# Kernel optimization log

Hardware: AMD Instinct MI355X
Metric: run time of the kernel (lower is better)

## Reference

```python
import jax, jax.numpy as jnp
import numpy as np

EPS = 1e-8
N_REFINE = 10
LR_REFINE = 0.1
N_SAMPLES = 12
M_BLEND = 0.3      # self.m
MARGIN = 0.2
TAU = 0.07
USE_INFONCE = True


def safe_norm(x, axis=-1):
    return x / jnp.clip(jnp.linalg.norm(x, axis=axis, keepdims=True), EPS, None)


def setup_inputs() -> dict:
    key = jax.random.key(0)
    k1, k2, k3, k4 = jax.random.split(key, 4)
    K, C, N, H, W = 10, 768, 8, 64, 64
    fg_proto = safe_norm(jax.random.normal(k1, (K, C), jnp.float32))
    bg_proto = safe_norm(jax.random.normal(k2, (K, C), jnp.float32))
    F_map = jax.random.normal(k3, (N, C, H, W), jnp.float32)
    M_map = jax.random.uniform(k4, (N, 1, H, W), jnp.float32)
    return {"fg_proto": fg_proto, "bg_proto": bg_proto, "F_map": F_map, "M_map": M_map}


def _refine(feats, p0):
    """Iterative spherical k-means style refinement.
    feats: [S, C] unit vectors (constants), p0: [K, C] centers.
    Vectorized segment-sum version of the per-cluster torch loop
    (updates within one iteration are independent across k)."""
    K = p0.shape[0]
    ones = jnp.ones((feats.shape[0],), feats.dtype)

    def body(p, it):
        step = LR_REFINE / (1.0 + 0.5 * it)
        assign = jnp.argmax(feats @ p.T, axis=1)                      # [S]
        sums = jax.ops.segment_sum(feats, assign, num_segments=K)    # [K, C]
        cnts = jax.ops.segment_sum(ones, assign, num_segments=K)     # [K]
        mean = sums / jnp.clip(cnts, 1.0, None)[:, None]
        new = safe_norm((1.0 - step) * p + step * mean)
        p = jnp.where((cnts > 0)[:, None], new, p)
        return p, None

    p, _ = jax.lax.scan(body, p0, jnp.arange(N_REFINE, dtype=p0.dtype))
    return p


def reference(fg_proto, bg_proto, F_map, M_map):
    N, C, H, W = F_map.shape
    # mask already at feature resolution -> nearest interpolate is identity
    M_flat = jnp.clip(M_map, 0.0, 1.0).reshape(-1)                   # [N*H*W]
    F_flat = safe_norm(jnp.transpose(F_map, (0, 2, 3, 1)).reshape(-1, C))

    # min cosine distance to any prototype == 1 - max similarity
    dist_fg_min = 1.0 - jnp.max(F_flat @ fg_proto.T, axis=1)
    dist_bg_min = 1.0 - jnp.max(F_flat @ bg_proto.T, axis=1)
    score_fg = jax.lax.stop_gradient(dist_fg_min * M_flat)
    score_bg = jax.lax.stop_gradient(dist_bg_min * (1.0 - M_flat))
    pos_idx = jax.lax.top_k(score_fg, N_SAMPLES)[1]
    neg_idx = jax.lax.top_k(score_bg, N_SAMPLES)[1]

    pos_feats = F_flat[pos_idx]                                       # [12, C]
    neg_feats = F_flat[neg_idx]

    # refinement runs under torch.no_grad on detached copies
    p_fg = _refine(jax.lax.stop_gradient(pos_feats), jax.lax.stop_gradient(fg_proto))
    p_bg = _refine(jax.lax.stop_gradient(neg_feats), jax.lax.stop_gradient(bg_proto))

    # triplet loss
    pos_n = safe_norm(pos_feats)
    neg_n = safe_norm(neg_feats)
    sim_pos = jnp.mean(jnp.max(pos_n @ p_fg.T, axis=1))
    sim_neg = jnp.mean(jnp.max(neg_n @ p_fg.T, axis=1))
    loss = jax.nn.relu(MARGIN + sim_neg - sim_pos)

    if USE_INFONCE:
        pos_sim = pos_n @ p_fg.T / TAU                                # [12, K]
        neg_sim = pos_n @ p_bg.T / TAU                                # [12, K]
        numer = jax.nn.logsumexp(pos_sim, axis=1)
        denom = jax.nn.logsumexp(jnp.concatenate([pos_sim, neg_sim], axis=1), axis=1)
        loss = loss + 0.25 * (-jnp.mean(numer - denom))

    refined_fg = safe_norm((1.0 - M_BLEND) * fg_proto + M_BLEND * p_fg)
    refined_bg = safe_norm((1.0 - M_BLEND) * bg_proto + M_BLEND * p_bg)
    return loss, refined_fg, refined_bg
```

## Files before the change

kernel.cpp:

```cpp
#include <hip/hip_runtime.h>
#include <math.h>

#define KP   10
#define CC   768
#define NB   8
#define HW   4096
#define STOT 32768
#define NS   12
#define NBLK 256
#define NREG 8

#define WS_CAND  0
#define WS_FEATS 12352
#define WS_PFG   30784
#define WS_PBG   38464

typedef unsigned long long ull;
typedef float f2v __attribute__((ext_vector_type(2)));

__device__ __forceinline__ f2v fma2(f2v a, float b, f2v c) {
#if __has_builtin(__builtin_elementwise_fma)
    f2v bb = b;
    return __builtin_elementwise_fma(a, bb, c);
#else
    f2v r; r.x = fmaf(a.x, b, c.x); r.y = fmaf(a.y, b, c.y); return r;
#endif
}

__device__ __forceinline__ float dpp_sum64(float x) {
#define DPP_ADD(ctrl) \
    x += __uint_as_float((unsigned)__builtin_amdgcn_update_dpp(0, (int)__float_as_uint(x), ctrl, 0xf, 0xf, true))
    DPP_ADD(0x111);
    DPP_ADD(0x112);
    DPP_ADD(0x114);
    DPP_ADD(0x118);
    DPP_ADD(0x142);
    DPP_ADD(0x143);
#undef DPP_ADD
    return x;
}
__device__ __forceinline__ float bcast63(float x) {
    return __uint_as_float((unsigned)__builtin_amdgcn_readlane((int)__float_as_uint(x), 63));
}

__device__ __forceinline__ ull pack_key(float v, int idx) {
    unsigned u = __float_as_uint(v);
    u ^= (unsigned)((int)u >> 31) | 0x80000000u;
    return ((ull)u << 32) | (ull)(0xFFFFFFFFu - (unsigned)idx);
}

__global__ __launch_bounds__(1024) void k_scores(const float* __restrict__ fg,
                                                 const float* __restrict__ bg,
                                                 const float* __restrict__ F,
                                                 const float* __restrict__ M,
                                                 ull* __restrict__ cand) {
    __shared__ float pl[20 * CC];
    __shared__ float part[8][64][2][21];
    __shared__ ull kfl[128], kbl[128];

    const int tid  = threadIdx.x;
    const int w    = __builtin_amdgcn_readfirstlane(tid >> 6);
    const int lane = tid & 63;
    const int b    = blockIdx.x;
    const int n    = b >> 5;
    const int hwb  = (b & 31) * 128 + lane * 2;
    const float* fp = F + ((size_t)n * CC) * HW + hwb;
    const int cbase = w * 48;

    f2v fnA[8], fnB[8];
#pragma unroll
    for (int j = 0; j < 8; ++j)
        fnA[j] = __builtin_nontemporal_load((const f2v*)(fp + (size_t)(cbase + j) * HW));
#pragma unroll
    for (int j = 0; j < 8; ++j)
        fnB[j] = __builtin_nontemporal_load((const f2v*)(fp + (size_t)(cbase + 8 + j) * HW));

    for (int i = tid; i < KP * CC; i += 1024) {
        pl[i]           = fg[i];
        pl[KP * CC + i] = bg[i];
    }
    __syncthreads();

    f2v afg[KP], abg[KP], n2;
#pragma unroll
    for (int k = 0; k < KP; ++k) { afg[k] = 0.f; abg[k] = 0.f; }
    n2 = 0.f;

    for (int c0 = 0; c0 < 48; c0 += 8) {
        f2v f[8];
#pragma unroll
        for (int j = 0; j < 8; ++j) { f[j] = fnA[j]; fnA[j] = fnB[j]; }
        if (c0 + 16 < 48) {
#pragma unroll
            for (int j = 0; j < 8; ++j)
                fnB[j] = __builtin_nontemporal_load((const f2v*)(fp + (size_t)(cbase + c0 + 16 + j) * HW));
        }

#pragma unroll
        for (int k = 0; k < KP; ++k) {
            const float4* pq = (const float4*)&pl[k * CC + cbase + c0];
            float4 a = pq[0], c = pq[1];
            f2v acc = afg[k];
            acc = fma2(f[0], a.x, acc); acc = fma2(f[1], a.y, acc);
            acc = fma2(f[2], a.z, acc); acc = fma2(f[3], a.w, acc);
            acc = fma2(f[4], c.x, acc); acc = fma2(f[5], c.y, acc);
            acc = fma2(f[6], c.z, acc); acc = fma2(f[7], c.w, acc);
            afg[k] = acc;
        }
#pragma unroll
        for (int k = 0; k < KP; ++k) {
            const float4* pq = (const float4*)&pl[(KP + k) * CC + cbase + c0];
            float4 a = pq[0], c = pq[1];
            f2v acc = abg[k];
            acc = fma2(f[0], a.x, acc); acc = fma2(f[1], a.y, acc);
            acc = fma2(f[2], a.z, acc); acc = fma2(f[3], a.w, acc);
            acc = fma2(f[4], c.x, acc); acc = fma2(f[5], c.y, acc);
            acc = fma2(f[6], c.z, acc); acc = fma2(f[7], c.w, acc);
            abg[k] = acc;
        }
#pragma unroll
        for (int j = 0; j < 8; ++j) {
#if __has_builtin(__builtin_elementwise_fma)
            n2 = __builtin_elementwise_fma(f[j], f[j], n2);
#else
            n2.x = fmaf(f[j].x, f[j].x, n2.x); n2.y = fmaf(f[j].y, f[j].y, n2.y);
#endif
        }
    }

    if (w >= 8) {
#pragma unroll
        for (int k = 0; k < KP; ++k) {
            part[w - 8][lane][0][k]      = afg[k].x; part[w - 8][lane][1][k]      = afg[k].y;
            part[w - 8][lane][0][10 + k] = abg[k].x; part[w - 8][lane][1][10 + k] = abg[k].y;
        }
        part[w - 8][lane][0][20] = n2.x; part[w - 8][lane][1][20] = n2.y;
    }
    __syncthreads();
    if (w < 8) {
#pragma unroll
        for (int k = 0; k < KP; ++k) {
            part[w][lane][0][k]      += afg[k].x; part[w][lane][1][k]      += afg[k].y;
            part[w][lane][0][10 + k] += abg[k].x; part[w][lane][1][10 + k] += abg[k].y;
        }
        part[w][lane][0][20] += n2.x; part[w][lane][1][20] += n2.y;
    }
    __syncthreads();

    if (tid < 128) {
        const int lane2 = tid >> 1, j = tid & 1;
        float vals[21];
#pragma unroll
        for (int q = 0; q < 21; ++q) {
            float acc = 0.f;
#pragma unroll
            for (int ss = 0; ss < 8; ++ss) acc += part[ss][lane2][j][q];
            vals[q] = acc;
        }
        float mfg = vals[0], mbg = vals[10];
#pragma unroll
        for (int k = 1; k < KP; ++k) { mfg = fmaxf(mfg, vals[k]); mbg = fmaxf(mbg, vals[10 + k]); }
        float nc = fmaxf(sqrtf(vals[20]), 1e-8f);
        int sp = b * 128 + tid;
        float m = fminf(fmaxf(M[sp], 0.f), 1.f);
        kfl[tid] = pack_key((1.f - mfg / nc) * m, sp);
        kbl[tid] = pack_key((1.f - mbg / nc) * (1.f - m), sp);
    }
    __syncthreads();

    if (w == 0) {
        ull k0 = kfl[lane], k1 = kfl[64 + lane];
        for (int r = 0; r < NS; ++r) {
            ull bk = (k0 > k1) ? k0 : k1;
#pragma unroll
            for (int m2 = 1; m2 < 64; m2 <<= 1) {
                ull o = __shfl_xor(bk, m2, 64);
                bk = (o > bk) ? o : bk;
            }
            if (lane == 0) cand[b * NS + r] = bk;
            if (k0 == bk) k0 = 0ull;
            if (k1 == bk) k1 = 0ull;
        }
    } else if (w == 1) {
        ull k0 = kbl[lane], k1 = kbl[64 + lane];
        for (int r = 0; r < NS; ++r) {
            ull bk = (k0 > k1) ? k0 : k1;
#pragma unroll
            for (int m2 = 1; m2 < 64; m2 <<= 1) {
                ull o = __shfl_xor(bk, m2, 64);
                bk = (o > bk) ? o : bk;
            }
            if (lane == 0) cand[NBLK * NS + b * NS + r] = bk;
            if (k0 == bk) k0 = 0ull;
            if (k1 == bk) k1 = 0ull;
        }
    }
}

__global__ __launch_bounds__(256) void k_gather(const ull* __restrict__ cand,
                                                const float* __restrict__ F,
                                                float* __restrict__ feats) {
    __shared__ int   sel_sh;
    __shared__ float red[256];

    const int b    = blockIdx.x;
    const int side = b / NS, row = b - side * NS;
    const int tid  = threadIdx.x;
    const int wave = tid >> 6, lane = tid & 63;

    if (wave == 0) {
        const ull* cs = cand + side * (NBLK * NS);
        ull tv[NS];
#pragma unroll
        for (int q = 0; q < NS; ++q) tv[q] = 0ull;
        for (int c = 0; c < 48; ++c) {
            ull key = cs[c * 64 + lane];
            if (key > tv[NS - 1]) {
#pragma unroll
                for (int q = NS - 1; q >= 1; --q) {
                    bool shift = key > tv[q - 1];
                    bool here  = !shift && (key > tv[q]);
                    tv[q] = shift ? tv[q - 1] : (here ? key : tv[q]);
                }
                if (key > tv[0]) tv[0] = key;
            }
        }
        ull win = 0ull;
        for (int r = 0; r <= row; ++r) {
            ull bk = tv[0];
#pragma unroll
            for (int m2 = 1; m2 < 64; m2 <<= 1) {
                ull o = __shfl_xor(bk, m2, 64);
                bk = (o > bk) ? o : bk;
            }
            if (r == row) win = bk;
            bool w0 = (tv[0] == bk);
#pragma unroll
            for (int q = 0; q < NS - 1; ++q) tv[q] = w0 ? tv[q + 1] : tv[q];
            tv[NS - 1] = w0 ? 0ull : tv[NS - 1];
        }
        if (lane == 0) sel_sh = (int)(0xFFFFFFFFu - (unsigned)(win & 0xFFFFFFFFull));
    }
    __syncthreads();

    const int sp = sel_sh;
    const float* fp = F + ((size_t)(sp >> 12) * CC) * HW + (sp & 4095);
    float v0 = fp[(size_t)(tid)       * HW];
    float v1 = fp[(size_t)(tid + 256) * HW];
    float v2 = fp[(size_t)(tid + 512) * HW];
    red[tid] = v0 * v0 + v1 * v1 + v2 * v2;
    __syncthreads();
    for (int off = 128; off > 0; off >>= 1) { if (tid < off) red[tid] += red[tid + off]; __syncthreads(); }
    float inv = 1.f / fmaxf(sqrtf(red[0]), 1e-8f);
    float* fo = feats + (side * NS + row) * CC;
    fo[tid]       = v0 * inv;
    fo[tid + 256] = v1 * inv;
    fo[tid + 512] = v2 * inv;
}

__global__ __launch_bounds__(640) void k_refine(const float* __restrict__ feats,
                                                const float* __restrict__ fg,
                                                const float* __restrict__ bg,
                                                float* __restrict__ pfg,
                                                float* __restrict__ pbg,
                                                float* __restrict__ out) {
    __shared__ float fe[NS * CC];
    __shared__ float dots[NS][KP];
    __shared__ int   assign[NS];

    const int side = blockIdx.x;
    const int tid  = threadIdx.x;
    const int wave = __builtin_amdgcn_readfirstlane(tid >> 6);
    const int lane = tid & 63;
    const int k    = wave;
    const float* p0 = (side == 0) ? fg : bg;
    float* pout     = (side == 0) ? pfg : pbg;

    {
        const float4* fi = (const float4*)(feats + side * (NS * CC));
        float4* fl = (float4*)fe;
        for (int i = tid; i < NS * CC / 4; i += 640) fl[i] = fi[i];
    }
    __syncthreads();

    float4 fer[NREG][3];
#pragma unroll
    for (int s = 0; s < NREG; ++s)
#pragma unroll
        for (int j4 = 0; j4 < 3; ++j4)
            fer[s][j4] = *(const float4*)&fe[s * CC + j4 * 256 + lane * 4];

    float4 p[3];
#pragma unroll
    for (int j4 = 0; j4 < 3; ++j4)
        p[j4] = *(const float4*)&p0[k * CC + j4 * 256 + lane * 4];

    for (int it = 0; it < 10; ++it) {
        float step = 0.1f / (1.0f + 0.5f * (float)it);

        float d[NS];
#pragma unroll
        for (int s = 0; s < NS; ++s) d[s] = 0.f;
#pragma unroll
        for (int j4 = 0; j4 < 3; ++j4) {
            float4 pv = p[j4];
#pragma unroll
            for (int s = 0; s < NREG; ++s) {
                float4 fv = fer[s][j4];
                d[s] = fmaf(fv.x, pv.x, d[s]);
                d[s] = fmaf(fv.y, pv.y, d[s]);
                d[s] = fmaf(fv.z, pv.z, d[s]);
                d[s] = fmaf(fv.w, pv.w, d[s]);
            }
#pragma unroll
            for (int s = NREG; s < NS; ++s) {
                float4 fv = *(const float4*)&fe[s * CC + j4 * 256 + lane * 4];
                d[s] = fmaf(fv.x, pv.x, d[s]);
                d[s] = fmaf(fv.y, pv.y, d[s]);
                d[s] = fmaf(fv.z, pv.z, d[s]);
                d[s] = fmaf(fv.w, pv.w, d[s]);
            }
        }
#pragma unroll
        for (int s = 0; s < NS; ++s) d[s] = dpp_sum64(d[s]);
        if (lane == 63) {
#pragma unroll
            for (int s = 0; s < NS; ++s) dots[s][k] = d[s];
        }
        __syncthreads();

        if (tid < NS) {
            float bv = dots[tid][0]; int bk = 0;
#pragma unroll
            for (int kk = 1; kk < KP; ++kk) { float v = dots[tid][kk]; if (v > bv) { bv = v; bk = kk; } }
            assign[tid] = bk;
        }
        __syncthreads();

        int a[NS]; int cnt = 0;
#pragma unroll
        for (int s = 0; s < NS; ++s) { a[s] = assign[s]; cnt += (a[s] == k) ? 1 : 0; }

        if (cnt > 0) {
            float4 mac[3];
#pragma unroll
            for (int j4 = 0; j4 < 3; ++j4) mac[j4] = make_float4(0.f, 0.f, 0.f, 0.f);
#pragma unroll
            for (int s = 0; s < NREG; ++s) {
                if (a[s] == k) {
#pragma unroll
                    for (int j4 = 0; j4 < 3; ++j4) {
                        float4 fv = fer[s][j4];
                        mac[j4].x += fv.x; mac[j4].y += fv.y; mac[j4].z += fv.z; mac[j4].w += fv.w;
                    }
                }
            }
#pragma unroll
            for (int s = NREG; s < NS; ++s) {
                if (a[s] == k) {
#pragma unroll
                    for (int j4 = 0; j4 < 3; ++j4) {
                        float4 fv = *(const float4*)&fe[s * CC + j4 * 256 + lane * 4];
                        mac[j4].x += fv.x; mac[j4].y += fv.y; mac[j4].z += fv.z; mac[j4].w += fv.w;
                    }
                }
            }
            float fcnt = (float)cnt;
            float4 v[3]; float ss = 0.f;
#pragma unroll
            for (int j4 = 0; j4 < 3; ++j4) {
                v[j4].x = (1.0f - step) * p[j4].x + step * (mac[j4].x / fcnt);
                v[j4].y = (1.0f - step) * p[j4].y + step * (mac[j4].y / fcnt);
                v[j4].z = (1.0f - step) * p[j4].z + step * (mac[j4].z / fcnt);
                v[j4].w = (1.0f - step) * p[j4].w + step * (mac[j4].w / fcnt);
                ss = fmaf(v[j4].x, v[j4].x, ss);
                ss = fmaf(v[j4].y, v[j4].y, ss);
                ss = fmaf(v[j4].z, v[j4].z, ss);
                ss = fmaf(v[j4].w, v[j4].w, ss);
            }
            float tot = bcast63(dpp_sum64(ss));
            float inv = 1.f / fmaxf(sqrtf(tot), 1e-8f);
#pragma unroll
            for (int j4 = 0; j4 < 3; ++j4) {
                p[j4].x = v[j4].x * inv; p[j4].y = v[j4].y * inv;
                p[j4].z = v[j4].z * inv; p[j4].w = v[j4].w * inv;
            }
        }
    }

#pragma unroll
    for (int j4 = 0; j4 < 3; ++j4)
        *(float4*)&pout[k * CC + j4 * 256 + lane * 4] = p[j4];

    float4 vv[3]; float ss2 = 0.f;
#pragma unroll
    for (int j4 = 0; j4 < 3; ++j4) {
        float4 pz = *(const float4*)&p0[k * CC + j4 * 256 + lane * 4];
        vv[j4].x = 0.7f * pz.x + 0.3f * p[j4].x;
        vv[j4].y = 0.7f * pz.y + 0.3f * p[j4].y;
        vv[j4].z = 0.7f * pz.z + 0.3f * p[j4].z;
        vv[j4].w = 0.7f * pz.w + 0.3f * p[j4].w;
        ss2 = fmaf(vv[j4].x, vv[j4].x, ss2);
        ss2 = fmaf(vv[j4].y, vv[j4].y, ss2);
        ss2 = fmaf(vv[j4].z, vv[j4].z, ss2);
        ss2 = fmaf(vv[j4].w, vv[j4].w, ss2);
    }
    float tot2 = bcast63(dpp_sum64(ss2));
    float inv2 = 1.f / fmaxf(sqrtf(tot2), 1e-8f);
    float* orow = out + 1 + (side * KP + k) * CC;
#pragma unroll
    for (int j4 = 0; j4 < 3; ++j4) {
        float4 o4;
        o4.x = vv[j4].x * inv2; o4.y = vv[j4].y * inv2;
        o4.z = vv[j4].z * inv2; o4.w = vv[j4].w * inv2;
        *(float4*)&orow[j4 * 256 + lane * 4] = o4;
    }
}

__global__ __launch_bounds__(1024) void k_loss(const float* __restrict__ feats,
                                               const float* __restrict__ pfg,
                                               const float* __restrict__ pbg,
                                               float* __restrict__ out) {
    __shared__ float dots3[NS * 30];
    __shared__ float mp[NS], mn[NS], infon[NS];
    int tid = threadIdx.x, wave = tid >> 6, lane = tid & 63;

    for (int pid = wave; pid < 360; pid += 16) {
        int g = pid / 120, rr = pid % 120, s = rr / KP, k = rr % KP;
        const float4* a4 = (const float4*)(feats + ((g == 1 ? NS + s : s) * CC) + lane * 12);
        const float4* b4 = (const float4*)((g == 2 ? pbg : pfg) + k * CC + lane * 12);
        float acc = 0.f;
#pragma unroll
        for (int j = 0; j < 3; ++j) {
            float4 a = a4[j], b = b4[j];
            acc += a.x * b.x + a.y * b.y + a.z * b.z + a.w * b.w;
        }
        acc = dpp_sum64(acc);
        if (lane == 63) dots3[s * 30 + g * 10 + k] = acc;
    }
    __syncthreads();

    if (tid < NS) {
        const float* d = &dots3[tid * 30];
        float maxp = d[0], maxn = d[10];
#pragma unroll
        for (int k = 1; k < KP; ++k) { maxp = fmaxf(maxp, d[k]); maxn = fmaxf(maxn, d[10 + k]); }
        mp[tid] = maxp; mn[tid] = maxn;

        float x[KP], y[KP];
#pragma unroll
        for (int k = 0; k < KP; ++k) { x[k] = d[k] / 0.07f; y[k] = d[20 + k] / 0.07f; }
        float m10 = x[0];
#pragma unroll
        for (int k = 1; k < KP; ++k) m10 = fmaxf(m10, x[k]);
        float se = 0.f;
#pragma unroll
        for (int k = 0; k < KP; ++k) se += expf(x[k] - m10);
        float numer = logf(se) + m10;
        float m20 = m10;
#pragma unroll
        for (int k = 0; k < KP; ++k) m20 = fmaxf(m20, y[k]);
        float se2 = 0.f;
#pragma unroll
        for (int k = 0; k < KP; ++k) se2 += expf(x[k] - m20);
#pragma unroll
        for (int k = 0; k < KP; ++k) se2 += expf(y[k] - m20);
        float denom = logf(se2) + m20;
        infon[tid] = numer - denom;
    }
    __syncthreads();
    if (tid == 0) {
        float sp = 0.f, sn = 0.f, si = 0.f;
        for (int s = 0; s < NS; ++s) { sp += mp[s]; sn += mn[s]; si += infon[s]; }
        sp /= 12.f; sn /= 12.f; si /= 12.f;
        float loss = fmaxf(0.2f + sn - sp, 0.f) + 0.25f * (-si);
        out[0] = loss;
    }
}

extern "C" void kernel_launch(void* const* d_in, const int* in_sizes, int n_in,
                              void* d_out, int out_size, void* d_ws, size_t ws_size,
                              hipStream_t stream) {
    const float* fg = (const float*)d_in[0];
    const float* bg = (const float*)d_in[1];
    const float* F  = (const float*)d_in[2];
    const float* M  = (const float*)d_in[3];
    float* out = (float*)d_out;

    float* w    = (float*)d_ws;
    ull*   cand = (ull*)(w + WS_CAND);
    float* fea  = w + WS_FEATS;
    float* pfg  = w + WS_PFG;
    float* pbg  = w + WS_PBG;

    k_scores<<<NBLK, 1024, 0, stream>>>(fg, bg, F, M, cand);
    k_gather<<<24, 256, 0, stream>>>(cand, F, fea);
    k_refine<<<2, 640, 0, stream>>>(fea, fg, bg, pfg, pbg, out);
    k_loss  <<<1, 1024, 0, stream>>>(fea, pfg, pbg, out);
}
```

Baseline: 111.2 us.

## Split score kernel into separate fg and bg block halves

The scoring kernel now launches twice as many blocks, with each block handling only the foreground or only the background prototypes. This halves the per-block accumulator registers and shared memory, which should allow more occupancy and give the small 256-block grid more parallelism across CUs. The cost is that the 100MB feature map is read twice (once per side) and the norm is computed twice, so the kernel may become more memory-bound.

```diff
diff --git a/kernel.cpp b/kernel.cpp
--- a/kernel.cpp
+++ b/kernel.cpp
@@ -49,23 +49,25 @@
     return ((ull)u << 32) | (ull)(0xFFFFFFFFu - (unsigned)idx);
 }
 
-__global__ __launch_bounds__(1024) void k_scores(const float* __restrict__ fg,
-                                                 const float* __restrict__ bg,
-                                                 const float* __restrict__ F,
-                                                 const float* __restrict__ M,
-                                                 ull* __restrict__ cand) {
-    __shared__ float pl[20 * CC];
-    __shared__ float part[8][64][2][21];
-    __shared__ ull kfl[128], kbl[128];
+__global__ __launch_bounds__(1024, 8) void k_scores(const float* __restrict__ fg,
+                                                    const float* __restrict__ bg,
+                                                    const float* __restrict__ F,
+                                                    const float* __restrict__ M,
+                                                    ull* __restrict__ cand) {
+    __shared__ float pl[KP * CC];
+    __shared__ float part[8][64][2][11];
+    __shared__ ull   kl[128];
 
     const int tid  = threadIdx.x;
     const int w    = __builtin_amdgcn_readfirstlane(tid >> 6);
     const int lane = tid & 63;
-    const int b    = blockIdx.x;
+    const int side = blockIdx.x >> 8;
+    const int b    = blockIdx.x & 255;
     const int n    = b >> 5;
     const int hwb  = (b & 31) * 128 + lane * 2;
     const float* fp = F + ((size_t)n * CC) * HW + hwb;
     const int cbase = w * 48;
+    const float* pr = (side == 0) ? fg : bg;
 
     f2v fnA[8], fnB[8];
 #pragma unroll
@@ -75,15 +77,16 @@
     for (int j = 0; j < 8; ++j)
         fnB[j] = __builtin_nontemporal_load((const f2v*)(fp + (size_t)(cbase + 8 + j) * HW));
 
-    for (int i = tid; i < KP * CC; i += 1024) {
-        pl[i]           = fg[i];
-        pl[KP * CC + i] = bg[i];
-    }
-    __syncthreads();
-
-    f2v afg[KP], abg[KP], n2;
-#pragma unroll
-    for (int k = 0; k < KP; ++k) { afg[k] = 0.f; abg[k] = 0.f; }
+    {
+        const float4* pr4 = (const float4*)pr;
+        float4* pl4 = (float4*)pl;
+        for (int i = tid; i < KP * CC / 4; i += 1024) pl4[i] = pr4[i];
+    }
+    __syncthreads();
+
+    f2v acc[KP], n2;
+#pragma unroll
+    for (int k = 0; k < KP; ++k) acc[k] = 0.f;
     n2 = 0.f;
 
     for (int c0 = 0; c0 < 48; c0 += 8) {
@@ -100,23 +103,12 @@
         for (int k = 0; k < KP; ++k) {
             const float4* pq = (const float4*)&pl[k * CC + cbase + c0];
             float4 a = pq[0], c = pq[1];
-            f2v acc = afg[k];
-            acc = fma2(f[0], a.x, acc); acc = fma2(f[1], a.y, acc);
-            acc = fma2(f[2], a.z, acc); acc = fma2(f[3], a.w, acc);
-            acc = fma2(f[4], c.x, acc); acc = fma2(f[5], c.y, acc);
-            acc = fma2(f[6], c.z, acc); acc = fma2(f[7], c.w, acc);
-            afg[k] = acc;
-        }
-#pragma unroll
-        for (int k = 0; k < KP; ++k) {
-            const float4* pq = (const float4*)&pl[(KP + k) * CC + cbase + c0];
-            float4 a = pq[0], c = pq[1];
-            f2v acc = abg[k];
-            acc = fma2(f[0], a.x, acc); acc = fma2(f[1], a.y, acc);
-            acc = fma2(f[2], a.z, acc); acc = fma2(f[3], a.w, acc);
-            acc = fma2(f[4], c.x, acc); acc = fma2(f[5], c.y, acc);
-            acc = fma2(f[6], c.z, acc); acc = fma2(f[7], c.w, acc);
-            abg[k] = acc;
+            f2v av = acc[k];
+            av = fma2(f[0], a.x, av); av = fma2(f[1], a.y, av);
+            av = fma2(f[2], a.z, av); av = fma2(f[3], a.w, av);
+            av = fma2(f[4], c.x, av); av = fma2(f[5], c.y, av);
+            av = fma2(f[6], c.z, av); av = fma2(f[7], c.w, av);
+            acc[k] = av;
         }
 #pragma unroll
         for (int j = 0; j < 8; ++j) {
@@ -131,45 +123,43 @@
     if (w >= 8) {
 #pragma unroll
         for (int k = 0; k < KP; ++k) {
-            part[w - 8][lane][0][k]      = afg[k].x; part[w - 8][lane][1][k]      = afg[k].y;
-            part[w - 8][lane][0][10 + k] = abg[k].x; part[w - 8][lane][1][10 + k] = abg[k].y;
-        }
-        part[w - 8][lane][0][20] = n2.x; part[w - 8][lane][1][20] = n2.y;
+            part[w - 8][lane][0][k] = acc[k].x; part[w - 8][lane][1][k] = acc[k].y;
+        }
+        part[w - 8][lane][0][10] = n2.x; part[w - 8][lane][1][10] = n2.y;
     }
     __syncthreads();
     if (w < 8) {
 #pragma unroll
         for (int k = 0; k < KP; ++k) {
-            part[w][lane][0][k]      += afg[k].x; part[w][lane][1][k]      += afg[k].y;
-            part[w][lane][0][10 + k] += abg[k].x; part[w][lane][1][10 + k] += abg[k].y;
-        }
-        part[w][lane][0][20] += n2.x; part[w][lane][1][20] += n2.y;
+            part[w][lane][0][k] += acc[k].x; part[w][lane][1][k] += acc[k].y;
+        }
+        part[w][lane][0][10] += n2.x; part[w][lane][1][10] += n2.y;
     }
     __syncthreads();
 
     if (tid < 128) {
         const int lane2 = tid >> 1, j = tid & 1;
-        float vals[21];
-#pragma unroll
-        for (int q = 0; q < 21; ++q) {
-            float acc = 0.f;
-#pragma unroll
-            for (int ss = 0; ss < 8; ++ss) acc += part[ss][lane2][j][q];
-            vals[q] = acc;
-        }
-        float mfg = vals[0], mbg = vals[10];
-#pragma unroll
-        for (int k = 1; k < KP; ++k) { mfg = fmaxf(mfg, vals[k]); mbg = fmaxf(mbg, vals[10 + k]); }
-        float nc = fmaxf(sqrtf(vals[20]), 1e-8f);
+        float vals[11];
+#pragma unroll
+        for (int q = 0; q < 11; ++q) {
+            float a2 = 0.f;
+#pragma unroll
+            for (int ss = 0; ss < 8; ++ss) a2 += part[ss][lane2][j][q];
+            vals[q] = a2;
+        }
+        float mx = vals[0];
+#pragma unroll
+        for (int k = 1; k < KP; ++k) mx = fmaxf(mx, vals[k]);
+        float nc = fmaxf(sqrtf(vals[10]), 1e-8f);
         int sp = b * 128 + tid;
         float m = fminf(fmaxf(M[sp], 0.f), 1.f);
-        kfl[tid] = pack_key((1.f - mfg / nc) * m, sp);
-        kbl[tid] = pack_key((1.f - mbg / nc) * (1.f - m), sp);
+        float wgt = (side == 0) ? m : (1.f - m);
+        kl[tid] = pack_key((1.f - mx / nc) * wgt, sp);
     }
     __syncthreads();
 
     if (w == 0) {
-        ull k0 = kfl[lane], k1 = kfl[64 + lane];
+        ull k0 = kl[lane], k1 = kl[64 + lane];
         for (int r = 0; r < NS; ++r) {
             ull bk = (k0 > k1) ? k0 : k1;
 #pragma unroll
@@ -177,20 +167,7 @@
                 ull o = __shfl_xor(bk, m2, 64);
                 bk = (o > bk) ? o : bk;
             }
-            if (lane == 0) cand[b * NS + r] = bk;
-            if (k0 == bk) k0 = 0ull;
-            if (k1 == bk) k1 = 0ull;
-        }
-    } else if (w == 1) {
-        ull k0 = kbl[lane], k1 = kbl[64 + lane];
-        for (int r = 0; r < NS; ++r) {
-            ull bk = (k0 > k1) ? k0 : k1;
-#pragma unroll
-            for (int m2 = 1; m2 < 64; m2 <<= 1) {
-                ull o = __shfl_xor(bk, m2, 64);
-                bk = (o > bk) ? o : bk;
-            }
-            if (lane == 0) cand[NBLK * NS + b * NS + r] = bk;
+            if (lane == 0) cand[side * (NBLK * NS) + b * NS + r] = bk;
             if (k0 == bk) k0 = 0ull;
             if (k1 == bk) k1 = 0ull;
         }
@@ -493,7 +470,7 @@
     float* pfg  = w + WS_PFG;
     float* pbg  = w + WS_PBG;
 
-    k_scores<<<NBLK, 1024, 0, stream>>>(fg, bg, F, M, cand);
+    k_scores<<<2 * NBLK, 1024, 0, stream>>>(fg, bg, F, M, cand);
     k_gather<<<24, 256, 0, stream>>>(cand, F, fea);
     k_refine<<<2, 640, 0, stream>>>(fea, fg, bg, pfg, pbg, out);
     k_loss  <<<1, 1024, 0, stream>>>(fea, pfg, pbg, out);
```

Measured after the change: 121.5 us. +9.3%, slower.
